# Performance work log

Measured on AMD Instinct MI355X. Metric: run time of the kernel, lower is better.

## Reference

```python
import jax, jax.numpy as jnp
import numpy as np

N = 100000      # nodes
E = 1200000     # edges (avg degree ~12)
D_IN = 64
D_OUT = 64


def setup_inputs() -> dict:
    key = jax.random.key(0)
    k1, k2, k3, k4 = jax.random.split(key, 4)
    x = jax.random.normal(k1, (N, D_IN), dtype=jnp.float32)
    # learned params (glorot-ish init)
    W = jax.random.normal(k2, (D_IN, D_OUT), dtype=jnp.float32) / np.sqrt(D_IN).astype(np.float32)
    b = jnp.zeros((D_OUT,), dtype=jnp.float32)
    src = jax.random.randint(k3, (E,), 0, N, dtype=jnp.int32)
    dst = jax.random.randint(k4, (E,), 0, N, dtype=jnp.int32)
    return {"x": x, "W": W, "b": b, "src": src, "dst": dst}


def reference(x, W, b, src, dst):
    # GCN layer: h = relu( D^-1/2 A D^-1/2 (x @ W) + b ), dropout=0 (eval)
    ones = jnp.ones(src.shape[0], dtype=x.dtype)
    deg_out = jax.ops.segment_sum(ones, src, num_segments=N)   # out-degree of source nodes
    deg_in = jax.ops.segment_sum(ones, dst, num_segments=N)    # in-degree of dest nodes
    norm_src = jax.lax.rsqrt(jnp.maximum(deg_out, 1.0))
    norm_dst = jax.lax.rsqrt(jnp.maximum(deg_in, 1.0))

    h = x @ W                                                  # [N, D_OUT] dense transform
    msg = h[src] * norm_src[src][:, None]                      # [E, D_OUT] gathered, pre-normalized messages
    agg = jax.ops.segment_sum(msg, dst, num_segments=N)        # [N, D_OUT] sparse aggregation
    out = agg * norm_dst[:, None] + b
    return jax.nn.relu(out)
```

## Files before the change

kernel.cpp:

```cpp
#include <hip/hip_runtime.h>
#include <hip/hip_bf16.h>

#define N_NODES 100000
#define N_EDGES 1200000
#define NPAIRS  (N_EDGES / 2)
#define DCH 64

typedef __attribute__((ext_vector_type(8))) short bf16x8;
typedef __attribute__((ext_vector_type(4))) float f32x4;

#define K1B 256
#define K1T 1024
#define NRID 8
#define RID_NODES 12500
#define RID_WORDS 3125
#define SLICE_PAIRS (NPAIRS / (K1B / NRID))
#define SCAT_PAIRS ((NPAIRS + K1B - 1) / K1B)

#define BNODES 128
#define KBUK ((N_NODES + BNODES - 1) / BNODES)
#define CAPE 3008
#define CAPN 40

#define K2B 128
#define K2T 512
#define NTILES (N_NODES / 16)
#define K2WAVES (K2B * K2T / 64)

#define K3T 512

#define OFF_DEG      0
#define OFF_GCUR     100096
#define OFF_FLAG     103296
#define OFF_ESORT    103424
#define OFF_HS       9512704

__device__ __forceinline__ float load_f(const void* p, int i, int f32) {
    if (f32) return ((const float*)p)[i];
    return __bfloat162float(((const __hip_bfloat16*)p)[i]);
}

__device__ __forceinline__ unsigned short f2bf_bits(float f) {
    __hip_bfloat16 h = __float2bfloat16(f);
    return __builtin_bit_cast(unsigned short, h);
}

__global__ __launch_bounds__(K1T, 4)
void edges_kernel(const int* __restrict__ src,
                  const int* __restrict__ dst,
                  const void* __restrict__ x,
                  unsigned int* __restrict__ deg_packed,
                  int* __restrict__ gcur,
                  unsigned int* __restrict__ esort,
                  int* __restrict__ flag) {
    __shared__ unsigned int h[RID_WORDS];
    __shared__ int cnt[KBUK];
    __shared__ int base[KBUK];
    __shared__ int cur[KBUK];
    int tid = threadIdx.x, bid = blockIdx.x;

    if (bid == 0) {
        if (tid == 0) h[0] = 0;
        __syncthreads();
        if (tid < 256) {
            const unsigned short* u = (const unsigned short*)x;
            int c = 0;
            for (int i = tid * 16; i < tid * 16 + 16; ++i) {
                unsigned short v = u[2 * i];
                int e = (v >> 7) & 0xFF;
                if (e >= 141) c++;
            }
            if (c) atomicAdd(&h[0], (unsigned int)c);
        }
        __syncthreads();
        if (tid == 0) *flag = (h[0] > 256) ? 1 : 0;
        __syncthreads();
    }

    {
        int rid = bid & (NRID - 1);
        int j   = bid >> 3;
        for (int w = tid; w < RID_WORDS; w += K1T) h[w] = 0;
        __syncthreads();
        int lo = rid * RID_NODES;
        const int2* s2 = (const int2*)src;
        int p0 = j * SLICE_PAIRS, p1 = p0 + SLICE_PAIRS;
        for (int p = p0 + tid; p < p1; p += K1T) {
            int2 sp = s2[p];
            int n0 = sp.x - lo, n1 = sp.y - lo;
            if ((unsigned)n0 < (unsigned)RID_NODES)
                atomicAdd(&h[n0 >> 2], 1u << ((n0 & 3) * 8));
            if ((unsigned)n1 < (unsigned)RID_NODES)
                atomicAdd(&h[n1 >> 2], 1u << ((n1 & 3) * 8));
        }
        __syncthreads();
        unsigned int* dp = deg_packed + rid * RID_WORDS;
        for (int w = tid; w < RID_WORDS; w += K1T) {
            unsigned int v = h[w];
            if (v) atomicAdd(&dp[w], v);
        }
    }

    {
        int p0 = bid * SCAT_PAIRS;
        int p1 = p0 + SCAT_PAIRS; if (p1 > NPAIRS) p1 = NPAIRS;
        const int2* s2 = (const int2*)src;
        const int2* d2 = (const int2*)dst;
        for (int i = tid; i < KBUK; i += K1T) { cnt[i] = 0; cur[i] = 0; }
        __syncthreads();
        for (int p = p0 + tid; p < p1; p += K1T) {
            int2 dp = d2[p];
            atomicAdd(&cnt[dp.x >> 7], 1);
            atomicAdd(&cnt[dp.y >> 7], 1);
        }
        __syncthreads();
        for (int i = tid; i < KBUK; i += K1T)
            if (cnt[i]) base[i] = atomicAdd(&gcur[i], cnt[i]);
        __syncthreads();
        for (int p = p0 + tid; p < p1; p += K1T) {
            int2 sp = s2[p];
            int2 dp = d2[p];
            int b0 = dp.x >> 7, b1 = dp.y >> 7;
            int pos0 = base[b0] + atomicAdd(&cur[b0], 1);
            if (pos0 < CAPE)
                esort[b0 * CAPE + pos0] =
                    (unsigned int)sp.x | ((unsigned int)(dp.x & 127) << 24);
            int pos1 = base[b1] + atomicAdd(&cur[b1], 1);
            if (pos1 < CAPE)
                esort[b1 * CAPE + pos1] =
                    (unsigned int)sp.y | ((unsigned int)(dp.y & 127) << 24);
        }
    }
}

__global__ __launch_bounds__(K2T, 4)
void gemm_kernel(const void* __restrict__ x,
                 const void* __restrict__ W,
                 const unsigned int* __restrict__ deg_packed,
                 __hip_bfloat16* __restrict__ hs) {
    __shared__ float wt[DCH * DCH];
    __shared__ int sn;
    int tid = threadIdx.x, bid = blockIdx.x;

    if (tid == 0) sn = 0;
    __syncthreads();
    if (tid < 256) {
        const unsigned short* u = (const unsigned short*)x;
        int c = 0;
        for (int i = tid * 16; i < tid * 16 + 16; ++i) {
            unsigned short v = u[2 * i];
            int e = (v >> 7) & 0xFF;
            if (e >= 141) c++;
        }
        if (c) atomicAdd(&sn, c);
    }
    __syncthreads();
    int f32 = sn > 256;

    for (int i = tid; i < DCH * DCH; i += K2T)
        wt[i] = load_f(W, i, f32);
    __syncthreads();

    int lane = tid & 63;
    int cB = lane & 15;
    int k0 = (lane >> 4) * 8;

    bf16x8 bf00, bf01, bf10, bf11, bf20, bf21, bf30, bf31;
#define LDB(DST, CT, KH) { bf16x8 t;                                      \
    _Pragma("unroll")                                                     \
    for (int j = 0; j < 8; ++j)                                           \
        t[j] = (short)f2bf_bits(wt[((KH)*32 + k0 + j) * DCH + (CT)*16 + cB]); \
    DST = t; }
    LDB(bf00, 0, 0) LDB(bf01, 0, 1)
    LDB(bf10, 1, 0) LDB(bf11, 1, 1)
    LDB(bf20, 2, 0) LDB(bf21, 2, 1)
    LDB(bf30, 3, 0) LDB(bf31, 3, 1)
#undef LDB

    int wid = bid * (K2T / 64) + (tid >> 6);
    int rowA = lane & 15;
    for (int t = wid; t < NTILES; t += K2WAVES) {
        int nbase = t << 4;
        int node = nbase + rowA;
        bf16x8 a0, a1;
        if (f32) {
            const float* xr = (const float*)x + node * DCH + k0;
            float4 p0 = *(const float4*)(xr);
            float4 p1 = *(const float4*)(xr + 4);
            float4 p2 = *(const float4*)(xr + 32);
            float4 p3 = *(const float4*)(xr + 36);
            a0[0] = (short)f2bf_bits(p0.x); a0[1] = (short)f2bf_bits(p0.y);
            a0[2] = (short)f2bf_bits(p0.z); a0[3] = (short)f2bf_bits(p0.w);
            a0[4] = (short)f2bf_bits(p1.x); a0[5] = (short)f2bf_bits(p1.y);
            a0[6] = (short)f2bf_bits(p1.z); a0[7] = (short)f2bf_bits(p1.w);
            a1[0] = (short)f2bf_bits(p2.x); a1[1] = (short)f2bf_bits(p2.y);
            a1[2] = (short)f2bf_bits(p2.z); a1[3] = (short)f2bf_bits(p2.w);
            a1[4] = (short)f2bf_bits(p3.x); a1[5] = (short)f2bf_bits(p3.y);
            a1[6] = (short)f2bf_bits(p3.z); a1[7] = (short)f2bf_bits(p3.w);
        } else {
            const short* xr = (const short*)x + node * DCH + k0;
            a0 = *(const bf16x8*)(xr);
            a1 = *(const bf16x8*)(xr + 32);
        }
        f32x4 ac0 = {0.f,0.f,0.f,0.f}, ac1 = {0.f,0.f,0.f,0.f};
        f32x4 ac2 = {0.f,0.f,0.f,0.f}, ac3 = {0.f,0.f,0.f,0.f};
        ac0 = __builtin_amdgcn_mfma_f32_16x16x32_bf16(a0, bf00, ac0, 0, 0, 0);
        ac1 = __builtin_amdgcn_mfma_f32_16x16x32_bf16(a0, bf10, ac1, 0, 0, 0);
        ac2 = __builtin_amdgcn_mfma_f32_16x16x32_bf16(a0, bf20, ac2, 0, 0, 0);
        ac3 = __builtin_amdgcn_mfma_f32_16x16x32_bf16(a0, bf30, ac3, 0, 0, 0);
        ac0 = __builtin_amdgcn_mfma_f32_16x16x32_bf16(a1, bf01, ac0, 0, 0, 0);
        ac1 = __builtin_amdgcn_mfma_f32_16x16x32_bf16(a1, bf11, ac1, 0, 0, 0);
        ac2 = __builtin_amdgcn_mfma_f32_16x16x32_bf16(a1, bf21, ac2, 0, 0, 0);
        ac3 = __builtin_amdgcn_mfma_f32_16x16x32_bf16(a1, bf31, ac3, 0, 0, 0);

        int rbase = nbase + (lane >> 4) * 4;
#pragma unroll
        for (int r = 0; r < 4; ++r) {
            int n = rbase + r;
            unsigned int dw = deg_packed[n >> 2];
            float dg = (float)((dw >> ((n & 3) * 8)) & 0xFFu);
            float nr = rsqrtf(fmaxf(dg, 1.0f));
            __hip_bfloat16* ho = hs + n * DCH + cB;
            ho[0]  = __float2bfloat16(ac0[r] * nr);
            ho[16] = __float2bfloat16(ac1[r] * nr);
            ho[32] = __float2bfloat16(ac2[r] * nr);
            ho[48] = __float2bfloat16(ac3[r] * nr);
        }
    }
}

__global__ __launch_bounds__(K3T, 6)
void gather_kernel(const __hip_bfloat16* __restrict__ hs,
                   const unsigned int* __restrict__ esort,
                   const int* __restrict__ gcur,
                   const void* __restrict__ b,
                   const int* __restrict__ flag,
                   void* __restrict__ out) {
    __shared__ unsigned int slots[BNODES * CAPN];
    __shared__ int cur[BNODES];
    int k = blockIdx.x, tid = threadIdx.x;
    int bbase = k * CAPE;
    int m = gcur[k];
    if (m > CAPE) m = CAPE;

    if (tid < BNODES) cur[tid] = 0;
    __syncthreads();
    for (int e = tid; e < m; e += K3T) {
        unsigned int w = esort[bbase + e];
        int r = w >> 24;
        int pos = atomicAdd(&cur[r], 1);
        if (pos < CAPN) slots[r * CAPN + pos] = w & 0xFFFFFFu;
    }
    __syncthreads();

    int f32 = *flag;
    int lane = tid & 63, wv = tid >> 6;
    int q = lane >> 4;
    int cg = lane & 15;
    const unsigned short* hsu = (const unsigned short*)hs;
    float b0 = load_f(b, cg * 4 + 0, f32);
    float b1 = load_f(b, cg * 4 + 1, f32);
    float b2 = load_f(b, cg * 4 + 2, f32);
    float b3 = load_f(b, cg * 4 + 3, f32);
    int nlo = k * BNODES;

#define ACC(ACCV, U) \
    (ACCV).x += __uint_as_float((U).x << 16); \
    (ACCV).y += __uint_as_float((U).x & 0xFFFF0000u); \
    (ACCV).z += __uint_as_float((U).y << 16); \
    (ACCV).w += __uint_as_float((U).y & 0xFFFF0000u);

    for (int base = wv; base < BNODES; base += 16) {
        int tA = base, tB = base + 8;
        int degA = cur[tA], degB = cur[tB];
        int dA = degA < CAPN ? degA : CAPN;
        int dB = degB < CAPN ? degB : CAPN;
        const unsigned int* eA = slots + tA * CAPN;
        const unsigned int* eB = slots + tB * CAPN;
        float4 aA0 = {0.f,0.f,0.f,0.f}, aA1 = {0.f,0.f,0.f,0.f};
        float4 aA2 = {0.f,0.f,0.f,0.f}, aA3 = {0.f,0.f,0.f,0.f};
        float4 aB0 = {0.f,0.f,0.f,0.f}, aB1 = {0.f,0.f,0.f,0.f};
        float4 aB2 = {0.f,0.f,0.f,0.f}, aB3 = {0.f,0.f,0.f,0.f};
        int dmax = dA > dB ? dA : dB;
        for (int j0 = 0; j0 < dmax; j0 += 16) {
            int i0 = j0 + q, i1 = j0 + 4 + q, i2 = j0 + 8 + q, i3 = j0 + 12 + q;
            unsigned int sA0 = (i0 < dA) ? eA[i0] : 0u;
            unsigned int sA1 = (i1 < dA) ? eA[i1] : 0u;
            unsigned int sA2 = (i2 < dA) ? eA[i2] : 0u;
            unsigned int sA3 = (i3 < dA) ? eA[i3] : 0u;
            unsigned int sB0 = (i0 < dB) ? eB[i0] : 0u;
            unsigned int sB1 = (i1 < dB) ? eB[i1] : 0u;
            unsigned int sB2 = (i2 < dB) ? eB[i2] : 0u;
            unsigned int sB3 = (i3 < dB) ? eB[i3] : 0u;
            uint2 uA0 = ((const uint2*)(hsu + sA0 * DCH))[cg];
            uint2 uA1 = ((const uint2*)(hsu + sA1 * DCH))[cg];
            uint2 uA2 = ((const uint2*)(hsu + sA2 * DCH))[cg];
            uint2 uA3 = ((const uint2*)(hsu + sA3 * DCH))[cg];
            uint2 uB0 = ((const uint2*)(hsu + sB0 * DCH))[cg];
            uint2 uB1 = ((const uint2*)(hsu + sB1 * DCH))[cg];
            uint2 uB2 = ((const uint2*)(hsu + sB2 * DCH))[cg];
            uint2 uB3 = ((const uint2*)(hsu + sB3 * DCH))[cg];
            if (i0 < dA) { ACC(aA0, uA0) }
            if (i1 < dA) { ACC(aA1, uA1) }
            if (i2 < dA) { ACC(aA2, uA2) }
            if (i3 < dA) { ACC(aA3, uA3) }
            if (i0 < dB) { ACC(aB0, uB0) }
            if (i1 < dB) { ACC(aB1, uB1) }
            if (i2 < dB) { ACC(aB2, uB2) }
            if (i3 < dB) { ACC(aB3, uB3) }
        }
        float4 oA, oB;
        oA.x = (aA0.x + aA1.x) + (aA2.x + aA3.x);
        oA.y = (aA0.y + aA1.y) + (aA2.y + aA3.y);
        oA.z = (aA0.z + aA1.z) + (aA2.z + aA3.z);
        oA.w = (aA0.w + aA1.w) + (aA2.w + aA3.w);
        oB.x = (aB0.x + aB1.x) + (aB2.x + aB3.x);
        oB.y = (aB0.y + aB1.y) + (aB2.y + aB3.y);
        oB.z = (aB0.z + aB1.z) + (aB2.z + aB3.z);
        oB.w = (aB0.w + aB1.w) + (aB2.w + aB3.w);
        oA.x += __shfl_xor(oA.x, 16); oA.y += __shfl_xor(oA.y, 16);
        oA.z += __shfl_xor(oA.z, 16); oA.w += __shfl_xor(oA.w, 16);
        oA.x += __shfl_xor(oA.x, 32); oA.y += __shfl_xor(oA.y, 32);
        oA.z += __shfl_xor(oA.z, 32); oA.w += __shfl_xor(oA.w, 32);
        oB.x += __shfl_xor(oB.x, 16); oB.y += __shfl_xor(oB.y, 16);
        oB.z += __shfl_xor(oB.z, 16); oB.w += __shfl_xor(oB.w, 16);
        oB.x += __shfl_xor(oB.x, 32); oB.y += __shfl_xor(oB.y, 32);
        oB.z += __shfl_xor(oB.z, 32); oB.w += __shfl_xor(oB.w, 32);
        int myNode = nlo + ((lane < 16) ? tA : tB);
        int myDeg  = (lane < 16) ? degA : degB;
        float4 o   = (lane < 16) ? oA : oB;
        if (lane < 32 && myNode < N_NODES) {
            float nrm = rsqrtf(fmaxf((float)myDeg, 1.0f));
            o.x = fmaxf(o.x * nrm + b0, 0.0f);
            o.y = fmaxf(o.y * nrm + b1, 0.0f);
            o.z = fmaxf(o.z * nrm + b2, 0.0f);
            o.w = fmaxf(o.w * nrm + b3, 0.0f);
            if (f32) {
                ((float4*)out)[myNode * 16 + cg] = o;
            } else {
                ushort4 s;
                s.x = f2bf_bits(o.x);
                s.y = f2bf_bits(o.y);
                s.z = f2bf_bits(o.z);
                s.w = f2bf_bits(o.w);
                ((ushort4*)out)[myNode * 16 + cg] = s;
            }
        }
    }
#undef ACC
}

extern "C" void kernel_launch(void* const* d_in, const int* in_sizes, int n_in,
                              void* d_out, int out_size, void* d_ws, size_t ws_size,
                              hipStream_t stream) {
    const void* x   = d_in[0];
    const void* W   = d_in[1];
    const void* b   = d_in[2];
    const int*  src = (const int*)d_in[3];
    const int*  dst = (const int*)d_in[4];

    char* ws = (char*)d_ws;
    unsigned int* deg_packed = (unsigned int*)(ws + OFF_DEG);
    int* gcur     = (int*)(ws + OFF_GCUR);
    int* flag     = (int*)(ws + OFF_FLAG);
    unsigned int* esort = (unsigned int*)(ws + OFF_ESORT);
    __hip_bfloat16* hs  = (__hip_bfloat16*)(ws + OFF_HS);

    (void)hipMemsetAsync(ws, 0, OFF_FLAG + 4, stream);

    edges_kernel<<<K1B, K1T, 0, stream>>>(
        src, dst, x, deg_packed, gcur, esort, flag);

    gemm_kernel<<<K2B, K2T, 0, stream>>>(x, W, deg_packed, hs);

    gather_kernel<<<KBUK, K3T, 0, stream>>>(hs, esort, gcur, b, flag, d_out);
}
```

Before: 165.6 us.

## Fuse GEMM into edge kernel and apply source norm during gather

The dense x@W transform moves into the edge-processing kernel, which removes one kernel launch and the dependency on finished degrees. The GEMM now writes unnormalised h. The source-degree normalisation moves into the gather kernel: each edge slot packs the 8-bit out-degree of its source, and an rsqrt lookup table in shared memory scales each message with an fma. This adds a deg_packed load per edge in the gather bucketing phase, and the fused kernel now shares one shared-memory buffer across its phases with extra barriers.

```diff
diff --git a/kernel.cpp b/kernel.cpp
--- a/kernel.cpp
+++ b/kernel.cpp
@@ -22,10 +22,8 @@
 #define CAPE 3008
 #define CAPN 40
 
-#define K2B 128
-#define K2T 512
 #define NTILES (N_NODES / 16)
-#define K2WAVES (K2B * K2T / 64)
+#define GWAVES (K1B * K1T / 64)
 
 #define K3T 512
 
@@ -46,38 +44,109 @@
 }
 
 __global__ __launch_bounds__(K1T, 4)
-void edges_kernel(const int* __restrict__ src,
+void fused_kernel(const int* __restrict__ src,
                   const int* __restrict__ dst,
                   const void* __restrict__ x,
+                  const void* __restrict__ W,
                   unsigned int* __restrict__ deg_packed,
                   int* __restrict__ gcur,
                   unsigned int* __restrict__ esort,
-                  int* __restrict__ flag) {
-    __shared__ unsigned int h[RID_WORDS];
-    __shared__ int cnt[KBUK];
-    __shared__ int base[KBUK];
-    __shared__ int cur[KBUK];
+                  int* __restrict__ flag,
+                  __hip_bfloat16* __restrict__ hs) {
+    __shared__ __align__(16) char smem[16384];
+    __shared__ int sn;
     int tid = threadIdx.x, bid = blockIdx.x;
 
-    if (bid == 0) {
-        if (tid == 0) h[0] = 0;
-        __syncthreads();
-        if (tid < 256) {
-            const unsigned short* u = (const unsigned short*)x;
-            int c = 0;
-            for (int i = tid * 16; i < tid * 16 + 16; ++i) {
-                unsigned short v = u[2 * i];
-                int e = (v >> 7) & 0xFF;
-                if (e >= 141) c++;
+    if (tid == 0) sn = 0;
+    __syncthreads();
+    if (tid < 256) {
+        const unsigned short* u = (const unsigned short*)x;
+        int c = 0;
+        for (int i = tid * 16; i < tid * 16 + 16; ++i) {
+            unsigned short v = u[2 * i];
+            int e = (v >> 7) & 0xFF;
+            if (e >= 141) c++;
+        }
+        if (c) atomicAdd(&sn, c);
+    }
+    __syncthreads();
+    int f32 = sn > 256;
+    if (bid == 0 && tid == 0) *flag = f32;
+
+    {
+        float* wt = (float*)smem;
+        for (int i = tid; i < DCH * DCH; i += K1T)
+            wt[i] = load_f(W, i, f32);
+        __syncthreads();
+
+        int lane = tid & 63;
+        int cB = lane & 15;
+        int k0 = (lane >> 4) * 8;
+
+        bf16x8 bf00, bf01, bf10, bf11, bf20, bf21, bf30, bf31;
+#define LDB(DST, CT, KH) { bf16x8 t;                                      \
+    _Pragma("unroll")                                                     \
+    for (int j = 0; j < 8; ++j)                                           \
+        t[j] = (short)f2bf_bits(wt[((KH)*32 + k0 + j) * DCH + (CT)*16 + cB]); \
+    DST = t; }
+        LDB(bf00, 0, 0) LDB(bf01, 0, 1)
+        LDB(bf10, 1, 0) LDB(bf11, 1, 1)
+        LDB(bf20, 2, 0) LDB(bf21, 2, 1)
+        LDB(bf30, 3, 0) LDB(bf31, 3, 1)
+#undef LDB
+
+        int wid = bid * (K1T / 64) + (tid >> 6);
+        int rowA = lane & 15;
+        for (int t = wid; t < NTILES; t += GWAVES) {
+            int nbase = t << 4;
+            int node = nbase + rowA;
+            bf16x8 a0, a1;
+            if (f32) {
+                const float* xr = (const float*)x + node * DCH + k0;
+                float4 p0 = *(const float4*)(xr);
+                float4 p1 = *(const float4*)(xr + 4);
+                float4 p2 = *(const float4*)(xr + 32);
+                float4 p3 = *(const float4*)(xr + 36);
+                a0[0] = (short)f2bf_bits(p0.x); a0[1] = (short)f2bf_bits(p0.y);
+                a0[2] = (short)f2bf_bits(p0.z); a0[3] = (short)f2bf_bits(p0.w);
+                a0[4] = (short)f2bf_bits(p1.x); a0[5] = (short)f2bf_bits(p1.y);
+                a0[6] = (short)f2bf_bits(p1.z); a0[7] = (short)f2bf_bits(p1.w);
+                a1[0] = (short)f2bf_bits(p2.x); a1[1] = (short)f2bf_bits(p2.y);
+                a1[2] = (short)f2bf_bits(p2.z); a1[3] = (short)f2bf_bits(p2.w);
+                a1[4] = (short)f2bf_bits(p3.x); a1[5] = (short)f2bf_bits(p3.y);
+                a1[6] = (short)f2bf_bits(p3.z); a1[7] = (short)f2bf_bits(p3.w);
+            } else {
+                const short* xr = (const short*)x + node * DCH + k0;
+                a0 = *(const bf16x8*)(xr);
+                a1 = *(const bf16x8*)(xr + 32);
             }
-            if (c) atomicAdd(&h[0], (unsigned int)c);
-        }
-        __syncthreads();
-        if (tid == 0) *flag = (h[0] > 256) ? 1 : 0;
-        __syncthreads();
-    }
+            f32x4 ac0 = {0.f,0.f,0.f,0.f}, ac1 = {0.f,0.f,0.f,0.f};
+            f32x4 ac2 = {0.f,0.f,0.f,0.f}, ac3 = {0.f,0.f,0.f,0.f};
+            ac0 = __builtin_amdgcn_mfma_f32_16x16x32_bf16(a0, bf00, ac0, 0, 0, 0);
+            ac1 = __builtin_amdgcn_mfma_f32_16x16x32_bf16(a0, bf10, ac1, 0, 0, 0);
+            ac2 = __builtin_amdgcn_mfma_f32_16x16x32_bf16(a0, bf20, ac2, 0, 0, 0);
+            ac3 = __builtin_amdgcn_mfma_f32_16x16x32_bf16(a0, bf30, ac3, 0, 0, 0);
+            ac0 = __builtin_amdgcn_mfma_f32_16x16x32_bf16(a1, bf01, ac0, 0, 0, 0);
+            ac1 = __builtin_amdgcn_mfma_f32_16x16x32_bf16(a1, bf11, ac1, 0, 0, 0);
+            ac2 = __builtin_amdgcn_mfma_f32_16x16x32_bf16(a1, bf21, ac2, 0, 0, 0);
+            ac3 = __builtin_amdgcn_mfma_f32_16x16x32_bf16(a1, bf31, ac3, 0, 0, 0);
+
+            int rbase = nbase + (lane >> 4) * 4;
+#pragma unroll
+            for (int r = 0; r < 4; ++r) {
+                int n = rbase + r;
+                __hip_bfloat16* ho = hs + n * DCH + cB;
+                ho[0]  = __float2bfloat16(ac0[r]);
+                ho[16] = __float2bfloat16(ac1[r]);
+                ho[32] = __float2bfloat16(ac2[r]);
+                ho[48] = __float2bfloat16(ac3[r]);
+            }
+        }
+    }
+    __syncthreads();
 
     {
+        unsigned int* h = (unsigned int*)smem;
         int rid = bid & (NRID - 1);
         int j   = bid >> 3;
         for (int w = tid; w < RID_WORDS; w += K1T) h[w] = 0;
@@ -99,9 +168,13 @@
             unsigned int v = h[w];
             if (v) atomicAdd(&dp[w], v);
         }
+        __syncthreads();
     }
 
     {
+        int* cnt  = (int*)smem;
+        int* base = cnt + KBUK;
+        int* cur  = base + KBUK;
         int p0 = bid * SCAT_PAIRS;
         int p1 = p0 + SCAT_PAIRS; if (p1 > NPAIRS) p1 = NPAIRS;
         const int2* s2 = (const int2*)src;
@@ -133,123 +206,33 @@
     }
 }
 
-__global__ __launch_bounds__(K2T, 4)
-void gemm_kernel(const void* __restrict__ x,
-                 const void* __restrict__ W,
-                 const unsigned int* __restrict__ deg_packed,
-                 __hip_bfloat16* __restrict__ hs) {
-    __shared__ float wt[DCH * DCH];
-    __shared__ int sn;
-    int tid = threadIdx.x, bid = blockIdx.x;
-
-    if (tid == 0) sn = 0;
-    __syncthreads();
-    if (tid < 256) {
-        const unsigned short* u = (const unsigned short*)x;
-        int c = 0;
-        for (int i = tid * 16; i < tid * 16 + 16; ++i) {
-            unsigned short v = u[2 * i];
-            int e = (v >> 7) & 0xFF;
-            if (e >= 141) c++;
-        }
-        if (c) atomicAdd(&sn, c);
-    }
-    __syncthreads();
-    int f32 = sn > 256;
-
-    for (int i = tid; i < DCH * DCH; i += K2T)
-        wt[i] = load_f(W, i, f32);
-    __syncthreads();
-
-    int lane = tid & 63;
-    int cB = lane & 15;
-    int k0 = (lane >> 4) * 8;
-
-    bf16x8 bf00, bf01, bf10, bf11, bf20, bf21, bf30, bf31;
-#define LDB(DST, CT, KH) { bf16x8 t;                                      \
-    _Pragma("unroll")                                                     \
-    for (int j = 0; j < 8; ++j)                                           \
-        t[j] = (short)f2bf_bits(wt[((KH)*32 + k0 + j) * DCH + (CT)*16 + cB]); \
-    DST = t; }
-    LDB(bf00, 0, 0) LDB(bf01, 0, 1)
-    LDB(bf10, 1, 0) LDB(bf11, 1, 1)
-    LDB(bf20, 2, 0) LDB(bf21, 2, 1)
-    LDB(bf30, 3, 0) LDB(bf31, 3, 1)
-#undef LDB
-
-    int wid = bid * (K2T / 64) + (tid >> 6);
-    int rowA = lane & 15;
-    for (int t = wid; t < NTILES; t += K2WAVES) {
-        int nbase = t << 4;
-        int node = nbase + rowA;
-        bf16x8 a0, a1;
-        if (f32) {
-            const float* xr = (const float*)x + node * DCH + k0;
-            float4 p0 = *(const float4*)(xr);
-            float4 p1 = *(const float4*)(xr + 4);
-            float4 p2 = *(const float4*)(xr + 32);
-            float4 p3 = *(const float4*)(xr + 36);
-            a0[0] = (short)f2bf_bits(p0.x); a0[1] = (short)f2bf_bits(p0.y);
-            a0[2] = (short)f2bf_bits(p0.z); a0[3] = (short)f2bf_bits(p0.w);
-            a0[4] = (short)f2bf_bits(p1.x); a0[5] = (short)f2bf_bits(p1.y);
-            a0[6] = (short)f2bf_bits(p1.z); a0[7] = (short)f2bf_bits(p1.w);
-            a1[0] = (short)f2bf_bits(p2.x); a1[1] = (short)f2bf_bits(p2.y);
-            a1[2] = (short)f2bf_bits(p2.z); a1[3] = (short)f2bf_bits(p2.w);
-            a1[4] = (short)f2bf_bits(p3.x); a1[5] = (short)f2bf_bits(p3.y);
-            a1[6] = (short)f2bf_bits(p3.z); a1[7] = (short)f2bf_bits(p3.w);
-        } else {
-            const short* xr = (const short*)x + node * DCH + k0;
-            a0 = *(const bf16x8*)(xr);
-            a1 = *(const bf16x8*)(xr + 32);
-        }
-        f32x4 ac0 = {0.f,0.f,0.f,0.f}, ac1 = {0.f,0.f,0.f,0.f};
-        f32x4 ac2 = {0.f,0.f,0.f,0.f}, ac3 = {0.f,0.f,0.f,0.f};
-        ac0 = __builtin_amdgcn_mfma_f32_16x16x32_bf16(a0, bf00, ac0, 0, 0, 0);
-        ac1 = __builtin_amdgcn_mfma_f32_16x16x32_bf16(a0, bf10, ac1, 0, 0, 0);
-        ac2 = __builtin_amdgcn_mfma_f32_16x16x32_bf16(a0, bf20, ac2, 0, 0, 0);
-        ac3 = __builtin_amdgcn_mfma_f32_16x16x32_bf16(a0, bf30, ac3, 0, 0, 0);
-        ac0 = __builtin_amdgcn_mfma_f32_16x16x32_bf16(a1, bf01, ac0, 0, 0, 0);
-        ac1 = __builtin_amdgcn_mfma_f32_16x16x32_bf16(a1, bf11, ac1, 0, 0, 0);
-        ac2 = __builtin_amdgcn_mfma_f32_16x16x32_bf16(a1, bf21, ac2, 0, 0, 0);
-        ac3 = __builtin_amdgcn_mfma_f32_16x16x32_bf16(a1, bf31, ac3, 0, 0, 0);
-
-        int rbase = nbase + (lane >> 4) * 4;
-#pragma unroll
-        for (int r = 0; r < 4; ++r) {
-            int n = rbase + r;
-            unsigned int dw = deg_packed[n >> 2];
-            float dg = (float)((dw >> ((n & 3) * 8)) & 0xFFu);
-            float nr = rsqrtf(fmaxf(dg, 1.0f));
-            __hip_bfloat16* ho = hs + n * DCH + cB;
-            ho[0]  = __float2bfloat16(ac0[r] * nr);
-            ho[16] = __float2bfloat16(ac1[r] * nr);
-            ho[32] = __float2bfloat16(ac2[r] * nr);
-            ho[48] = __float2bfloat16(ac3[r] * nr);
-        }
-    }
-}
-
 __global__ __launch_bounds__(K3T, 6)
 void gather_kernel(const __hip_bfloat16* __restrict__ hs,
                    const unsigned int* __restrict__ esort,
                    const int* __restrict__ gcur,
+                   const unsigned int* __restrict__ deg_packed,
                    const void* __restrict__ b,
                    const int* __restrict__ flag,
                    void* __restrict__ out) {
     __shared__ unsigned int slots[BNODES * CAPN];
     __shared__ int cur[BNODES];
+    __shared__ float tab[256];
     int k = blockIdx.x, tid = threadIdx.x;
     int bbase = k * CAPE;
     int m = gcur[k];
     if (m > CAPE) m = CAPE;
 
     if (tid < BNODES) cur[tid] = 0;
+    if (tid < 256) tab[tid] = rsqrtf(fmaxf((float)tid, 1.0f));
     __syncthreads();
     for (int e = tid; e < m; e += K3T) {
         unsigned int w = esort[bbase + e];
         int r = w >> 24;
+        unsigned int s = w & 0xFFFFFFu;
+        unsigned int dw = deg_packed[s >> 2];
+        unsigned int degb = (dw >> ((s & 3) * 8)) & 0xFFu;
         int pos = atomicAdd(&cur[r], 1);
-        if (pos < CAPN) slots[r * CAPN + pos] = w & 0xFFFFFFu;
+        if (pos < CAPN) slots[r * CAPN + pos] = s | (degb << 24);
     }
     __syncthreads();
 
@@ -264,11 +247,11 @@
     float b3 = load_f(b, cg * 4 + 3, f32);
     int nlo = k * BNODES;
 
-#define ACC(ACCV, U) \
-    (ACCV).x += __uint_as_float((U).x << 16); \
-    (ACCV).y += __uint_as_float((U).x & 0xFFFF0000u); \
-    (ACCV).z += __uint_as_float((U).y << 16); \
-    (ACCV).w += __uint_as_float((U).y & 0xFFFF0000u);
+#define ACC(ACCV, U, F) \
+    (ACCV).x = fmaf(__uint_as_float((U).x << 16),         (F), (ACCV).x); \
+    (ACCV).y = fmaf(__uint_as_float((U).x & 0xFFFF0000u), (F), (ACCV).y); \
+    (ACCV).z = fmaf(__uint_as_float((U).y << 16),         (F), (ACCV).z); \
+    (ACCV).w = fmaf(__uint_as_float((U).y & 0xFFFF0000u), (F), (ACCV).w);
 
     for (int base = wv; base < BNODES; base += 16) {
         int tA = base, tB = base + 8;
@@ -284,30 +267,34 @@
         int dmax = dA > dB ? dA : dB;
         for (int j0 = 0; j0 < dmax; j0 += 16) {
             int i0 = j0 + q, i1 = j0 + 4 + q, i2 = j0 + 8 + q, i3 = j0 + 12 + q;
-            unsigned int sA0 = (i0 < dA) ? eA[i0] : 0u;
-            unsigned int sA1 = (i1 < dA) ? eA[i1] : 0u;
-            unsigned int sA2 = (i2 < dA) ? eA[i2] : 0u;
-            unsigned int sA3 = (i3 < dA) ? eA[i3] : 0u;
-            unsigned int sB0 = (i0 < dB) ? eB[i0] : 0u;
-            unsigned int sB1 = (i1 < dB) ? eB[i1] : 0u;
-            unsigned int sB2 = (i2 < dB) ? eB[i2] : 0u;
-            unsigned int sB3 = (i3 < dB) ? eB[i3] : 0u;
-            uint2 uA0 = ((const uint2*)(hsu + sA0 * DCH))[cg];
-            uint2 uA1 = ((const uint2*)(hsu + sA1 * DCH))[cg];
-            uint2 uA2 = ((const uint2*)(hsu + sA2 * DCH))[cg];
-            uint2 uA3 = ((const uint2*)(hsu + sA3 * DCH))[cg];
-            uint2 uB0 = ((const uint2*)(hsu + sB0 * DCH))[cg];
-            uint2 uB1 = ((const uint2*)(hsu + sB1 * DCH))[cg];
-            uint2 uB2 = ((const uint2*)(hsu + sB2 * DCH))[cg];
-            uint2 uB3 = ((const uint2*)(hsu + sB3 * DCH))[cg];
-            if (i0 < dA) { ACC(aA0, uA0) }
-            if (i1 < dA) { ACC(aA1, uA1) }
-            if (i2 < dA) { ACC(aA2, uA2) }
-            if (i3 < dA) { ACC(aA3, uA3) }
-            if (i0 < dB) { ACC(aB0, uB0) }
-            if (i1 < dB) { ACC(aB1, uB1) }
-            if (i2 < dB) { ACC(aB2, uB2) }
-            if (i3 < dB) { ACC(aB3, uB3) }
+            unsigned int wA0 = (i0 < dA) ? eA[i0] : 0u;
+            unsigned int wA1 = (i1 < dA) ? eA[i1] : 0u;
+            unsigned int wA2 = (i2 < dA) ? eA[i2] : 0u;
+            unsigned int wA3 = (i3 < dA) ? eA[i3] : 0u;
+            unsigned int wB0 = (i0 < dB) ? eB[i0] : 0u;
+            unsigned int wB1 = (i1 < dB) ? eB[i1] : 0u;
+            unsigned int wB2 = (i2 < dB) ? eB[i2] : 0u;
+            unsigned int wB3 = (i3 < dB) ? eB[i3] : 0u;
+            uint2 uA0 = ((const uint2*)(hsu + (wA0 & 0xFFFFFFu) * DCH))[cg];
+            uint2 uA1 = ((const uint2*)(hsu + (wA1 & 0xFFFFFFu) * DCH))[cg];
+            uint2 uA2 = ((const uint2*)(hsu + (wA2 & 0xFFFFFFu) * DCH))[cg];
+            uint2 uA3 = ((const uint2*)(hsu + (wA3 & 0xFFFFFFu) * DCH))[cg];
+            uint2 uB0 = ((const uint2*)(hsu + (wB0 & 0xFFFFFFu) * DCH))[cg];
+            uint2 uB1 = ((const uint2*)(hsu + (wB1 & 0xFFFFFFu) * DCH))[cg];
+            uint2 uB2 = ((const uint2*)(hsu + (wB2 & 0xFFFFFFu) * DCH))[cg];
+            uint2 uB3 = ((const uint2*)(hsu + (wB3 & 0xFFFFFFu) * DCH))[cg];
+            float fA0 = tab[wA0 >> 24], fA1 = tab[wA1 >> 24];
+            float fA2 = tab[wA2 >> 24], fA3 = tab[wA3 >> 24];
+            float fB0 = tab[wB0 >> 24], fB1 = tab[wB1 >> 24];
+            float fB2 = tab[wB2 >> 24], fB3 = tab[wB3 >> 24];
+            if (i0 < dA) { ACC(aA0, uA0, fA0) }
+            if (i1 < dA) { ACC(aA1, uA1, fA1) }
+            if (i2 < dA) { ACC(aA2, uA2, fA2) }
+            if (i3 < dA) { ACC(aA3, uA3, fA3) }
+            if (i0 < dB) { ACC(aB0, uB0, fB0) }
+            if (i1 < dB) { ACC(aB1, uB1, fB1) }
+            if (i2 < dB) { ACC(aB2, uB2, fB2) }
+            if (i3 < dB) { ACC(aB3, uB3, fB3) }
         }
         float4 oA, oB;
         oA.x = (aA0.x + aA1.x) + (aA2.x + aA3.x);
@@ -368,10 +355,9 @@
 
     (void)hipMemsetAsync(ws, 0, OFF_FLAG + 4, stream);
 
-    edges_kernel<<<K1B, K1T, 0, stream>>>(
-        src, dst, x, deg_packed, gcur, esort, flag);
-
-    gemm_kernel<<<K2B, K2T, 0, stream>>>(x, W, deg_packed, hs);
-
-    gather_kernel<<<KBUK, K3T, 0, stream>>>(hs, esort, gcur, b, flag, d_out);
-}
+    fused_kernel<<<K1B, K1T, 0, stream>>>(
+        src, dst, x, W, deg_packed, gcur, esort, flag, hs);
+
+    gather_kernel<<<KBUK, K3T, 0, stream>>>(
+        hs, esort, gcur, deg_packed, b, flag, d_out);
+}
```

Measured after the change: 153.1 us, median of 3. -7.5%, faster.
